# Performance work log

Measured on AMD Instinct MI355X. Metric: run time of the kernel, lower is better.

The kernel has to match this reference:

```python
import jax, jax.numpy as jnp
import numpy as np

N, E = 50000, 800000
IN_DIM, HID, HEADS, NUM_CLASSES, NUM_GRAPHS, NUM_LAYERS = 64, 64, 4, 10000, 256, 3
OUT_W = HID * HEADS  # 256


def _gat_layer(x, src, dst, W, a_src, a_dst, b, n_nodes):
    # x: [N, in], W: [heads*out, in], a_src/a_dst: [heads, out], b: [heads*out]
    h = (x @ W.T).reshape(n_nodes, HEADS, HID)            # [N, H, D]
    s_src = jnp.einsum('nhd,hd->nh', h, a_src)            # [N, H]
    s_dst = jnp.einsum('nhd,hd->nh', h, a_dst)
    alpha = jax.nn.leaky_relu(s_src[src] + s_dst[dst], 0.2)  # [E, H]
    m = jax.ops.segment_max(alpha, dst, num_segments=n_nodes)
    m = jnp.where(jnp.isfinite(m), m, 0.0)                # isolated-node safety
    ex = jnp.exp(alpha - m[dst])
    denom = jax.ops.segment_sum(ex, dst, num_segments=n_nodes)
    w = ex / (denom[dst] + 1e-16)                         # PyG softmax epsilon
    out = jax.ops.segment_sum(h[src] * w[:, :, None], dst, num_segments=n_nodes)
    return out.reshape(n_nodes, HEADS * HID) + b


def setup_inputs() -> dict:
    key = jax.random.key(0)
    ks = jax.random.split(key, 20)
    inp = {
        'x': jax.random.normal(ks[0], (N, IN_DIM), jnp.float32),
        'edge_index': jax.random.randint(ks[1], (2, E), 0, N, jnp.int32),
        'batch': jnp.sort(jax.random.randint(ks[2], (N,), 0, NUM_GRAPHS, jnp.int32)),
        'class_label': jax.random.randint(ks[3], (NUM_GRAPHS,), 0, NUM_CLASSES, jnp.int32),
        'emb': jax.random.normal(ks[4], (NUM_CLASSES, HID), jnp.float32),
    }
    in_dims = [IN_DIM + HID, OUT_W, OUT_W]
    for l in range(NUM_LAYERS):
        kw = jax.random.split(ks[5 + l], 4)
        d_in = in_dims[l]
        sc = 1.0 / np.sqrt(d_in)
        inp[f'W{l}'] = jax.random.uniform(kw[0], (OUT_W, d_in), jnp.float32, -sc, sc)
        inp[f'asrc{l}'] = jax.random.uniform(kw[1], (HEADS, HID), jnp.float32, -sc, sc)
        inp[f'adst{l}'] = jax.random.uniform(kw[2], (HEADS, HID), jnp.float32, -sc, sc)
        inp[f'b{l}'] = jnp.zeros((OUT_W,), jnp.float32)
    sc = 1.0 / np.sqrt(OUT_W)
    inp['cls_W'] = jax.random.uniform(ks[10], (1, OUT_W), jnp.float32, -sc, sc)
    inp['cls_b'] = jnp.zeros((1,), jnp.float32)
    return inp


def reference(x, edge_index, batch, class_label, emb,
              W0, asrc0, adst0, b0,
              W1, asrc1, adst1, b1,
              W2, asrc2, adst2, b2,
              cls_W, cls_b):
    n = x.shape[0]
    # template embedding aligned per node
    t = emb[class_label][batch]                          # [N, HID]
    h = jnp.concatenate([x, t], axis=-1)                 # [N, IN+HID]
    # PyG GATConv adds self-loops by default
    loop = jnp.arange(n, dtype=edge_index.dtype)
    src = jnp.concatenate([edge_index[0], loop])
    dst = jnp.concatenate([edge_index[1], loop])
    params = [(W0, asrc0, adst0, b0), (W1, asrc1, adst1, b1), (W2, asrc2, adst2, b2)]
    for (W, a_s, a_d, b) in params:
        h = _gat_layer(h, src, dst, W, a_s, a_d, b, n)
        h = jax.nn.leaky_relu(h, 0.01)                   # F.leaky_relu default slope
    return h @ cls_W.T + cls_b                           # [N, 1]
```

## Files before the change

### kernel.cpp

```cpp
#include <hip/hip_runtime.h>
#include <hip/hip_fp16.h>
#include <math.h>
#include <stdint.h>

#define NNODES 50000
#define NEDGES 800000
#define NT_TILES (((NNODES + 127) / 128) * 2)
#define NAGG_BLOCKS 2048
#define NAGG_WAVES (NAGG_BLOCKS * 4)
#define NH0 (NNODES * 128)
#define NH04 (NH0 / 4)
#define NW4 (163840 / 4)
#define NDEG4 (NNODES / 4)
#define NPREP4 (NH04 + NW4 + NDEG4)

typedef __attribute__((ext_vector_type(8))) _Float16 f16x8;
typedef __attribute__((ext_vector_type(4))) _Float16 f16x4;
typedef __attribute__((ext_vector_type(4))) float f32x4;

static __device__ __forceinline__ void gl_lds16(const void* g, void* l) {
    __builtin_amdgcn_global_load_lds(
        (const __attribute__((address_space(1))) void*)g,
        (__attribute__((address_space(3))) void*)l, 16, 0, 0);
}

static __device__ __forceinline__ float sel4(float4 v, int head) {
    float r = v.x;
    r = (head == 1) ? v.y : r;
    r = (head == 2) ? v.z : r;
    r = (head == 3) ? v.w : r;
    return r;
}

__global__ void prep_kernel(const float* __restrict__ x,
                            const int* __restrict__ batch,
                            const int* __restrict__ class_label,
                            const float* __restrict__ emb,
                            const float* __restrict__ W0,
                            const float* __restrict__ W1,
                            const float* __restrict__ W2,
                            _Float16* __restrict__ h0,
                            _Float16* __restrict__ F0,
                            _Float16* __restrict__ F1,
                            _Float16* __restrict__ F2,
                            int* __restrict__ deg) {
    int i4 = blockIdx.x * blockDim.x + threadIdx.x;
    if (i4 < NH04) {
        int idx = i4 * 4;
        int n = idx >> 7, c = idx & 127;
        float4 v;
        if (c < 64) v = *(const float4*)&x[(n << 6) + c];
        else        v = *(const float4*)&emb[class_label[batch[n]] * 64 + (c - 64)];
        f16x4 h = {(_Float16)v.x, (_Float16)v.y, (_Float16)v.z, (_Float16)v.w};
        *(f16x4*)&h0[idx] = h;
    } else if (i4 < NH04 + NW4) {
        int i = (i4 - NH04) * 4;
        const float* src; _Float16* dst;
        if (i < 32768)       { src = W0 + i;           dst = F0 + i; }
        else if (i < 98304)  { src = W1 + (i - 32768); dst = F1 + (i - 32768); }
        else                 { src = W2 + (i - 98304); dst = F2 + (i - 98304); }
        float4 v = *(const float4*)src;
        f16x4 h = {(_Float16)v.x, (_Float16)v.y, (_Float16)v.z, (_Float16)v.w};
        *(f16x4*)dst = h;
    } else if (i4 < NPREP4) {
        int j = (i4 - NH04 - NW4) * 4;
        int4 z = {0, 0, 0, 0};
        *(int4*)&deg[j] = z;
    }
}

template <int K>
static __device__ void gemm_tile_dev(const _Float16* __restrict__ A,
                                     const _Float16* __restrict__ W,
                                     const float* __restrict__ a_src,
                                     const float* __restrict__ a_dst,
                                     _Float16* __restrict__ Cf,
                                     float* __restrict__ ssrc,
                                     float* __restrict__ sdst,
                                     char* smem, int bm, int bn) {
    const int M = NNODES;
    int tid = threadIdx.x;
    int lane = tid & 63, wave = tid >> 6;
    int wm = wave >> 1, wn = wave & 1;
    int l16 = lane & 15, quad = lane >> 4;
    int rsub = lane >> 3;
    int kcs = (lane & 7) ^ rsub;
    int sw = l16 & 7;

    f32x4 acc[4][4];
#pragma unroll
    for (int r = 0; r < 4; ++r)
#pragma unroll
        for (int c = 0; c < 4; ++c) acc[r][c] = (f32x4){0.f, 0.f, 0.f, 0.f};

    const int NST = K / 64;
    auto issue = [&](int buf, int s) {
        _Float16* dA = (_Float16*)(smem + buf * 32768);
        _Float16* dB = (_Float16*)(smem + buf * 32768 + 16384);
        int ks = s * 64;
#pragma unroll
        for (int j = 0; j < 4; ++j) {
            int seg = wave * 4 + j;
            int r = seg * 8 + rsub;
            int acol = ks + kcs * 8;
            int garow = bm + r; if (garow > M - 1) garow = M - 1;
            gl_lds16(A + (size_t)garow * K + acol, &dA[seg * 512]);
            gl_lds16(W + (size_t)(bn + r) * K + acol, &dB[seg * 512]);
        }
    };

    issue(0, 0);
    __syncthreads();
#pragma unroll
    for (int s = 0; s < NST; ++s) {
        if (s + 1 < NST) issue((s + 1) & 1, s + 1);
        const _Float16* sA = (const _Float16*)(smem + (s & 1) * 32768);
        const _Float16* sB = (const _Float16*)(smem + (s & 1) * 32768 + 16384);
#pragma unroll
        for (int ks32 = 0; ks32 < 2; ++ks32) {
            f16x8 af[4], bf[4];
#pragma unroll
            for (int r = 0; r < 4; ++r) {
                int row = wm * 64 + r * 16 + l16;
                af[r] = *(const f16x8*)&sA[row * 64 + ((ks32 * 4 + quad) ^ sw) * 8];
            }
#pragma unroll
            for (int c = 0; c < 4; ++c) {
                int row = wn * 64 + c * 16 + l16;
                bf[c] = *(const f16x8*)&sB[row * 64 + ((ks32 * 4 + quad) ^ sw) * 8];
            }
#pragma unroll
            for (int r = 0; r < 4; ++r)
#pragma unroll
                for (int c = 0; c < 4; ++c)
                    acc[r][c] = __builtin_amdgcn_mfma_f32_16x16x32_f16(
                        bf[c], af[r], acc[r][c], 0, 0, 0);
        }
        __syncthreads();
    }

    int headblk = (bn + wn * 64) >> 6;
    f32x4 av[4], dv[4];
#pragma unroll
    for (int c = 0; c < 4; ++c) {
        av[c] = *(const f32x4*)&a_src[headblk * 64 + c * 16 + quad * 4];
        dv[c] = *(const f32x4*)&a_dst[headblk * 64 + c * 16 + quad * 4];
    }
#pragma unroll
    for (int r = 0; r < 4; ++r) {
        int grow = bm + wm * 64 + r * 16 + l16;
        bool ok = grow < M;
        float ps = 0.f, pd = 0.f;
#pragma unroll
        for (int c = 0; c < 4; ++c) {
            f32x4 a = acc[r][c];
            ps += a[0] * av[c][0] + a[1] * av[c][1]
                + a[2] * av[c][2] + a[3] * av[c][3];
            pd += a[0] * dv[c][0] + a[1] * dv[c][1]
                + a[2] * dv[c][2] + a[3] * dv[c][3];
            if (ok) {
                f16x4 hv = {(_Float16)a[0], (_Float16)a[1],
                            (_Float16)a[2], (_Float16)a[3]};
                *(f16x4*)&Cf[(size_t)grow * 256 + bn + wn * 64 + c * 16 + quad * 4] = hv;
            }
        }
        ps += __shfl_xor(ps, 16, 64);
        ps += __shfl_xor(ps, 32, 64);
        pd += __shfl_xor(pd, 16, 64);
        pd += __shfl_xor(pd, 32, 64);
        if (quad == 0 && ok) {
            ssrc[grow * 4 + headblk] = ps;
            sdst[grow * 4 + headblk] = pd;
        }
    }
}

template <int K>
__global__ __launch_bounds__(256) void gemm_mfma_kernel(
        const _Float16* __restrict__ A, const _Float16* __restrict__ W,
        const float* __restrict__ a_src, const float* __restrict__ a_dst,
        _Float16* __restrict__ Cf,
        float* __restrict__ ssrc, float* __restrict__ sdst) {
    __shared__ __align__(16) char smem[65536];
    gemm_tile_dev<K>(A, W, a_src, a_dst, Cf, ssrc, sdst, smem,
                     blockIdx.x * 128, blockIdx.y * 128);
}

__global__ __launch_bounds__(256) void gemm0_bucket_kernel(
        const _Float16* __restrict__ A, const _Float16* __restrict__ W,
        const float* __restrict__ a_src, const float* __restrict__ a_dst,
        _Float16* __restrict__ Cf,
        float* __restrict__ ssrc, float* __restrict__ sdst,
        const int* __restrict__ ei,
        int* __restrict__ deg, int* __restrict__ slots) {
    __shared__ __align__(16) char smem[65536];
    int b = blockIdx.x;
    if ((b & 1) == 0) {
        int tile = b >> 1;
        if (tile < NT_TILES)
            gemm_tile_dev<128>(A, W, a_src, a_dst, Cf, ssrc, sdst, smem,
                               (tile >> 1) * 128, (tile & 1) * 128);
    } else {
        int rel = b >> 1;
        int stride = NT_TILES * 256;
        for (int e = rel * 256 + (int)threadIdx.x; e < NEDGES; e += stride) {
            int d = ei[NEDGES + e];
            int pos = atomicAdd(&deg[d], 1);
            if (pos < 64) slots[(size_t)d * 64 + pos] = ei[e] << 9;
        }
    }
}

template <bool LAST>
__global__ __launch_bounds__(256) void aggregate_kernel(
        const _Float16* __restrict__ hpf,
        const float* __restrict__ ssrc,
        const float* __restrict__ sdst,
        const int* __restrict__ deg,
        const int* __restrict__ slots,
        const float* __restrict__ bias,
        _Float16* __restrict__ out_h,
        const float* __restrict__ cls_W,
        const float* __restrict__ cls_b,
        float* __restrict__ out) {
    __shared__ __align__(16) float s_w[4][64][4];
    __shared__ int s_idx[4][64];
    int lane = threadIdx.x & 63;
    int slot = threadIdx.x >> 6;
    int wid = blockIdx.x * 4 + slot;
    int head = lane >> 4;
    uint32_t lane8 = (uint32_t)lane * 8u;
    const char* hbase = (const char*)hpf;

    float4 bv = ((const float4*)bias)[lane];
    float4 wv = LAST ? ((const float4*)cls_W)[lane] : (float4){0.f, 0.f, 0.f, 0.f};

    for (int n = wid; n < NNODES; n += NAGG_WAVES) {
        int dn = deg[n]; if (dn > 64) dn = 64;
        float4 sd = ((const float4*)sdst)[n];

        float4 ssl = ((const float4*)ssrc)[n];
        float ax = ssl.x + sd.x, ay = ssl.y + sd.y;
        float az = ssl.z + sd.z, aw = ssl.w + sd.w;
        ax = ax > 0.f ? ax : 0.2f * ax;
        ay = ay > 0.f ? ay : 0.2f * ay;
        az = az > 0.f ? az : 0.2f * az;
        aw = aw > 0.f ? aw : 0.2f * aw;
        float4 exs = {__expf(ax), __expf(ay), __expf(az), __expf(aw)};
        float wself = sel4(exs, head);
        f16x4 vs = *(const f16x4*)(hbase + (((uint32_t)n << 9) + lane8));
        float dsum = wself;
        float4 acc = {wself * (float)vs.x, wself * (float)vs.y,
                      wself * (float)vs.z, wself * (float)vs.w};

        float4 ex = {0.f, 0.f, 0.f, 0.f};
        int soff = 0;
        if (lane < dn) {
            soff = slots[(size_t)n * 64 + lane];
            float4 ss = *(const float4*)((const char*)ssrc + ((uint32_t)soff >> 5));
            float bx = ss.x + sd.x, by = ss.y + sd.y;
            float bz = ss.z + sd.z, bw = ss.w + sd.w;
            bx = bx > 0.f ? bx : 0.2f * bx;
            by = by > 0.f ? by : 0.2f * by;
            bz = bz > 0.f ? bz : 0.2f * bz;
            bw = bw > 0.f ? bw : 0.2f * bw;
            ex.x = __expf(bx); ex.y = __expf(by);
            ex.z = __expf(bz); ex.w = __expf(bw);
        }
        *(float4*)&s_w[slot][lane][0] = ex;
        s_idx[slot][lane] = soff;

        int e = 0;
        for (; e + 8 <= dn; e += 8) {
            int si[8]; float w[8]; f16x4 v[8];
#pragma unroll
            for (int t = 0; t < 8; ++t) {
                si[t] = s_idx[slot][e + t];
                w[t] = s_w[slot][e + t][head];
            }
#pragma unroll
            for (int t = 0; t < 8; ++t)
                v[t] = *(const f16x4*)(hbase + ((uint32_t)si[t] + lane8));
#pragma unroll
            for (int t = 0; t < 8; ++t) {
                dsum += w[t];
                acc.x += w[t] * (float)v[t].x;
                acc.y += w[t] * (float)v[t].y;
                acc.z += w[t] * (float)v[t].z;
                acc.w += w[t] * (float)v[t].w;
            }
        }
        for (; e < dn; ++e) {
            int si = s_idx[slot][e];
            float w = s_w[slot][e][head];
            f16x4 v = *(const f16x4*)(hbase + ((uint32_t)si + lane8));
            dsum += w;
            acc.x += w * (float)v.x; acc.y += w * (float)v.y;
            acc.z += w * (float)v.z; acc.w += w * (float)v.w;
        }

        float inv = 1.f / (dsum + 1e-16f);
        float4 o;
        o.x = acc.x * inv + bv.x;
        o.y = acc.y * inv + bv.y;
        o.z = acc.z * inv + bv.z;
        o.w = acc.w * inv + bv.w;
        o.x = o.x > 0.f ? o.x : 0.01f * o.x;
        o.y = o.y > 0.f ? o.y : 0.01f * o.y;
        o.z = o.z > 0.f ? o.z : 0.01f * o.z;
        o.w = o.w > 0.f ? o.w : 0.01f * o.w;

        if (!LAST) {
            f16x4 ov = {(_Float16)o.x, (_Float16)o.y, (_Float16)o.z, (_Float16)o.w};
            ((f16x4*)out_h)[(size_t)n * 64 + lane] = ov;
        } else {
            float sdot = o.x * wv.x + o.y * wv.y + o.z * wv.z + o.w * wv.w;
#pragma unroll
            for (int off = 1; off < 64; off <<= 1)
                sdot += __shfl_xor(sdot, off, 64);
            if (lane == 0) out[n] = sdot + cls_b[0];
        }
    }
}

extern "C" void kernel_launch(void* const* d_in, const int* in_sizes, int n_in,
                              void* d_out, int out_size, void* d_ws, size_t ws_size,
                              hipStream_t stream) {
    const float* x     = (const float*)d_in[0];
    const int*   ei    = (const int*)d_in[1];
    const int*   batch = (const int*)d_in[2];
    const int*   clab  = (const int*)d_in[3];
    const float* emb   = (const float*)d_in[4];
    const float* W[3]    = {(const float*)d_in[5], (const float*)d_in[9],  (const float*)d_in[13]};
    const float* asrc[3] = {(const float*)d_in[6], (const float*)d_in[10], (const float*)d_in[14]};
    const float* adst[3] = {(const float*)d_in[7], (const float*)d_in[11], (const float*)d_in[15]};
    const float* bias[3] = {(const float*)d_in[8], (const float*)d_in[12], (const float*)d_in[16]};
    const float* clsW = (const float*)d_in[17];
    const float* clsb = (const float*)d_in[18];
    float* out = (float*)d_out;

    char* ws = (char*)d_ws;
    size_t off = 0;
    auto alloc = [&](size_t bytes) {
        void* p = ws + off;
        off += (bytes + 255) & ~(size_t)255;
        return p;
    };
    _Float16* Cf   = (_Float16*)alloc((size_t)NNODES * 256 * 2);
    _Float16* hA   = (_Float16*)alloc((size_t)NNODES * 256 * 2);
    _Float16* h0f  = (_Float16*)alloc((size_t)NNODES * 128 * 2);
    _Float16* Wf[3];
    Wf[0] = (_Float16*)alloc((size_t)256 * 128 * 2);
    Wf[1] = (_Float16*)alloc((size_t)256 * 256 * 2);
    Wf[2] = (_Float16*)alloc((size_t)256 * 256 * 2);
    float* ssrc  = (float*)alloc((size_t)NNODES * 4 * 4);
    float* sdst  = (float*)alloc((size_t)NNODES * 4 * 4);
    int*   deg   = (int*)alloc((size_t)NNODES * 4);
    int*   slots = (int*)alloc((size_t)NNODES * 64 * 4);
    (void)ws_size; (void)in_sizes; (void)n_in; (void)out_size;

    prep_kernel<<<dim3((NPREP4 + 255) / 256), dim3(256), 0, stream>>>(
        x, batch, clab, emb, W[0], W[1], W[2], h0f, Wf[0], Wf[1], Wf[2], deg);

    dim3 gemm_grid((NNODES + 127) / 128, 2);
    dim3 node_grid(NAGG_BLOCKS);

    gemm0_bucket_kernel<<<dim3(NT_TILES * 2), dim3(256), 0, stream>>>(
        h0f, Wf[0], asrc[0], adst[0], Cf, ssrc, sdst, ei, deg, slots);
    aggregate_kernel<false><<<node_grid, dim3(256), 0, stream>>>(
        Cf, ssrc, sdst, deg, slots, bias[0], hA, nullptr, nullptr, nullptr);

    gemm_mfma_kernel<256><<<gemm_grid, dim3(256), 0, stream>>>(
        hA, Wf[1], asrc[1], adst[1], Cf, ssrc, sdst);
    aggregate_kernel<false><<<node_grid, dim3(256), 0, stream>>>(
        Cf, ssrc, sdst, deg, slots, bias[1], hA, nullptr, nullptr, nullptr);

    gemm_mfma_kernel<256><<<gemm_grid, dim3(256), 0, stream>>>(
        hA, Wf[2], asrc[2], adst[2], Cf, ssrc, sdst);
    aggregate_kernel<true><<<node_grid, dim3(256), 0, stream>>>(
        Cf, ssrc, sdst, deg, slots, bias[2], nullptr, clsW, clsb, out);
}
```

Measured before the change: 384.0 us.

## Use atomic work-stealing queues over node ranges in aggregate kernel

After: 852.9 us. +122.1%, slower.

```diff
diff --git a/kernel.cpp b/kernel.cpp
--- a/kernel.cpp
+++ b/kernel.cpp
@@ -7,12 +7,14 @@
 #define NEDGES 800000
 #define NT_TILES (((NNODES + 127) / 128) * 2)
 #define NAGG_BLOCKS 2048
-#define NAGG_WAVES (NAGG_BLOCKS * 4)
+#define NRANGE 6250
+#define QCHUNK 4
 #define NH0 (NNODES * 128)
 #define NH04 (NH0 / 4)
 #define NW4 (163840 / 4)
 #define NDEG4 (NNODES / 4)
-#define NPREP4 (NH04 + NW4 + NDEG4)
+#define NCTR4 96
+#define NPREP4 (NH04 + NW4 + NDEG4 + NCTR4)
 
 typedef __attribute__((ext_vector_type(8))) _Float16 f16x8;
 typedef __attribute__((ext_vector_type(4))) _Float16 f16x4;
@@ -43,7 +45,8 @@
                             _Float16* __restrict__ F0,
                             _Float16* __restrict__ F1,
                             _Float16* __restrict__ F2,
-                            int* __restrict__ deg) {
+                            int* __restrict__ deg,
+                            int* __restrict__ ctr) {
     int i4 = blockIdx.x * blockDim.x + threadIdx.x;
     if (i4 < NH04) {
         int idx = i4 * 4;
@@ -62,10 +65,14 @@
         float4 v = *(const float4*)src;
         f16x4 h = {(_Float16)v.x, (_Float16)v.y, (_Float16)v.z, (_Float16)v.w};
         *(f16x4*)dst = h;
-    } else if (i4 < NPREP4) {
+    } else if (i4 < NH04 + NW4 + NDEG4) {
         int j = (i4 - NH04 - NW4) * 4;
         int4 z = {0, 0, 0, 0};
         *(int4*)&deg[j] = z;
+    } else if (i4 < NPREP4) {
+        int j = (i4 - NH04 - NW4 - NDEG4) * 4;
+        int4 z = {0, 0, 0, 0};
+        *(int4*)&ctr[j] = z;
     }
 }
 
@@ -222,7 +229,8 @@
         _Float16* __restrict__ out_h,
         const float* __restrict__ cls_W,
         const float* __restrict__ cls_b,
-        float* __restrict__ out) {
+        float* __restrict__ out,
+        int* __restrict__ ctr) {
     __shared__ __align__(16) float s_w[4][64][4];
     __shared__ int s_idx[4][64];
     int lane = threadIdx.x & 63;
@@ -234,91 +242,106 @@
 
     float4 bv = ((const float4*)bias)[lane];
     float4 wv = LAST ? ((const float4*)cls_W)[lane] : (float4){0.f, 0.f, 0.f, 0.f};
-
-    for (int n = wid; n < NNODES; n += NAGG_WAVES) {
-        int dn = deg[n]; if (dn > 64) dn = 64;
-        float4 sd = ((const float4*)sdst)[n];
-
-        float4 ssl = ((const float4*)ssrc)[n];
-        float ax = ssl.x + sd.x, ay = ssl.y + sd.y;
-        float az = ssl.z + sd.z, aw = ssl.w + sd.w;
-        ax = ax > 0.f ? ax : 0.2f * ax;
-        ay = ay > 0.f ? ay : 0.2f * ay;
-        az = az > 0.f ? az : 0.2f * az;
-        aw = aw > 0.f ? aw : 0.2f * aw;
-        float4 exs = {__expf(ax), __expf(ay), __expf(az), __expf(aw)};
-        float wself = sel4(exs, head);
-        f16x4 vs = *(const f16x4*)(hbase + (((uint32_t)n << 9) + lane8));
-        float dsum = wself;
-        float4 acc = {wself * (float)vs.x, wself * (float)vs.y,
-                      wself * (float)vs.z, wself * (float)vs.w};
-
-        float4 ex = {0.f, 0.f, 0.f, 0.f};
-        int soff = 0;
-        if (lane < dn) {
-            soff = slots[(size_t)n * 64 + lane];
-            float4 ss = *(const float4*)((const char*)ssrc + ((uint32_t)soff >> 5));
-            float bx = ss.x + sd.x, by = ss.y + sd.y;
-            float bz = ss.z + sd.z, bw = ss.w + sd.w;
-            bx = bx > 0.f ? bx : 0.2f * bx;
-            by = by > 0.f ? by : 0.2f * by;
-            bz = bz > 0.f ? bz : 0.2f * bz;
-            bw = bw > 0.f ? bw : 0.2f * bw;
-            ex.x = __expf(bx); ex.y = __expf(by);
-            ex.z = __expf(bz); ex.w = __expf(bw);
-        }
-        *(float4*)&s_w[slot][lane][0] = ex;
-        s_idx[slot][lane] = soff;
-
-        int e = 0;
-        for (; e + 8 <= dn; e += 8) {
-            int si[8]; float w[8]; f16x4 v[8];
-#pragma unroll
-            for (int t = 0; t < 8; ++t) {
-                si[t] = s_idx[slot][e + t];
-                w[t] = s_w[slot][e + t][head];
+    float cb = 0.f;
+    if (LAST) cb = cls_b[0];
+
+    int g0 = wid & 7;
+    for (int k = 0; k < 8; ++k) {
+        int g = (g0 + k) & 7;
+        int rbase = g * NRANGE;
+        for (;;) {
+            int b0 = 0;
+            if (lane == 0) b0 = atomicAdd(&ctr[g * 16], QCHUNK);
+            b0 = __shfl(b0, 0, 64);
+            if (b0 >= NRANGE) break;
+            int n1 = rbase + b0 + QCHUNK;
+            for (int n = rbase + b0; n < n1; ++n) {
+                int dn = deg[n]; if (dn > 64) dn = 64;
+                float4 sd = ((const float4*)sdst)[n];
+
+                float4 ssl = ((const float4*)ssrc)[n];
+                float ax = ssl.x + sd.x, ay = ssl.y + sd.y;
+                float az = ssl.z + sd.z, aw = ssl.w + sd.w;
+                ax = ax > 0.f ? ax : 0.2f * ax;
+                ay = ay > 0.f ? ay : 0.2f * ay;
+                az = az > 0.f ? az : 0.2f * az;
+                aw = aw > 0.f ? aw : 0.2f * aw;
+                float4 exs = {__expf(ax), __expf(ay), __expf(az), __expf(aw)};
+                float wself = sel4(exs, head);
+                f16x4 vs = *(const f16x4*)(hbase + (((uint32_t)n << 9) + lane8));
+                float dsum = wself;
+                float4 acc = {wself * (float)vs.x, wself * (float)vs.y,
+                              wself * (float)vs.z, wself * (float)vs.w};
+
+                float4 ex = {0.f, 0.f, 0.f, 0.f};
+                int soff = 0;
+                if (lane < dn) {
+                    soff = slots[(size_t)n * 64 + lane];
+                    float4 ss = *(const float4*)((const char*)ssrc + ((uint32_t)soff >> 5));
+                    float bx = ss.x + sd.x, by = ss.y + sd.y;
+                    float bz = ss.z + sd.z, bw = ss.w + sd.w;
+                    bx = bx > 0.f ? bx : 0.2f * bx;
+                    by = by > 0.f ? by : 0.2f * by;
+                    bz = bz > 0.f ? bz : 0.2f * bz;
+                    bw = bw > 0.f ? bw : 0.2f * bw;
+                    ex.x = __expf(bx); ex.y = __expf(by);
+                    ex.z = __expf(bz); ex.w = __expf(bw);
+                }
+                *(float4*)&s_w[slot][lane][0] = ex;
+                s_idx[slot][lane] = soff;
+
+                int e = 0;
+                for (; e + 8 <= dn; e += 8) {
+                    int si[8]; float w[8]; f16x4 v[8];
+#pragma unroll
+                    for (int t = 0; t < 8; ++t) {
+                        si[t] = s_idx[slot][e + t];
+                        w[t] = s_w[slot][e + t][head];
+                    }
+#pragma unroll
+                    for (int t = 0; t < 8; ++t)
+                        v[t] = *(const f16x4*)(hbase + ((uint32_t)si[t] + lane8));
+#pragma unroll
+                    for (int t = 0; t < 8; ++t) {
+                        dsum += w[t];
+                        acc.x += w[t] * (float)v[t].x;
+                        acc.y += w[t] * (float)v[t].y;
+                        acc.z += w[t] * (float)v[t].z;
+                        acc.w += w[t] * (float)v[t].w;
+                    }
+                }
+                for (; e < dn; ++e) {
+                    int si = s_idx[slot][e];
+                    float w = s_w[slot][e][head];
+                    f16x4 v = *(const f16x4*)(hbase + ((uint32_t)si + lane8));
+                    dsum += w;
+                    acc.x += w * (float)v.x; acc.y += w * (float)v.y;
+                    acc.z += w * (float)v.z; acc.w += w * (float)v.w;
+                }
+
+                float inv = 1.f / (dsum + 1e-16f);
+                float4 o;
+                o.x = acc.x * inv + bv.x;
+                o.y = acc.y * inv + bv.y;
+                o.z = acc.z * inv + bv.z;
+                o.w = acc.w * inv + bv.w;
+                o.x = o.x > 0.f ? o.x : 0.01f * o.x;
+                o.y = o.y > 0.f ? o.y : 0.01f * o.y;
+                o.z = o.z > 0.f ? o.z : 0.01f * o.z;
+                o.w = o.w > 0.f ? o.w : 0.01f * o.w;
+
+                if (!LAST) {
+                    f16x4 ov = {(_Float16)o.x, (_Float16)o.y,
+                                (_Float16)o.z, (_Float16)o.w};
+                    ((f16x4*)out_h)[(size_t)n * 64 + lane] = ov;
+                } else {
+                    float sdot = o.x * wv.x + o.y * wv.y + o.z * wv.z + o.w * wv.w;
+#pragma unroll
+                    for (int off = 1; off < 64; off <<= 1)
+                        sdot += __shfl_xor(sdot, off, 64);
+                    if (lane == 0) out[n] = sdot + cb;
+                }
             }
-#pragma unroll
-            for (int t = 0; t < 8; ++t)
-                v[t] = *(const f16x4*)(hbase + ((uint32_t)si[t] + lane8));
-#pragma unroll
-            for (int t = 0; t < 8; ++t) {
-                dsum += w[t];
-                acc.x += w[t] * (float)v[t].x;
-                acc.y += w[t] * (float)v[t].y;
-                acc.z += w[t] * (float)v[t].z;
-                acc.w += w[t] * (float)v[t].w;
-            }
-        }
-        for (; e < dn; ++e) {
-            int si = s_idx[slot][e];
-            float w = s_w[slot][e][head];
-            f16x4 v = *(const f16x4*)(hbase + ((uint32_t)si + lane8));
-            dsum += w;
-            acc.x += w * (float)v.x; acc.y += w * (float)v.y;
-            acc.z += w * (float)v.z; acc.w += w * (float)v.w;
-        }
-
-        float inv = 1.f / (dsum + 1e-16f);
-        float4 o;
-        o.x = acc.x * inv + bv.x;
-        o.y = acc.y * inv + bv.y;
-        o.z = acc.z * inv + bv.z;
-        o.w = acc.w * inv + bv.w;
-        o.x = o.x > 0.f ? o.x : 0.01f * o.x;
-        o.y = o.y > 0.f ? o.y : 0.01f * o.y;
-        o.z = o.z > 0.f ? o.z : 0.01f * o.z;
-        o.w = o.w > 0.f ? o.w : 0.01f * o.w;
-
-        if (!LAST) {
-            f16x4 ov = {(_Float16)o.x, (_Float16)o.y, (_Float16)o.z, (_Float16)o.w};
-            ((f16x4*)out_h)[(size_t)n * 64 + lane] = ov;
-        } else {
-            float sdot = o.x * wv.x + o.y * wv.y + o.z * wv.z + o.w * wv.w;
-#pragma unroll
-            for (int off = 1; off < 64; off <<= 1)
-                sdot += __shfl_xor(sdot, off, 64);
-            if (lane == 0) out[n] = sdot + cls_b[0];
         }
     }
 }
@@ -357,10 +380,11 @@
     float* sdst  = (float*)alloc((size_t)NNODES * 4 * 4);
     int*   deg   = (int*)alloc((size_t)NNODES * 4);
     int*   slots = (int*)alloc((size_t)NNODES * 64 * 4);
+    int*   ctr   = (int*)alloc((size_t)3 * 128 * 4);
     (void)ws_size; (void)in_sizes; (void)n_in; (void)out_size;
 
     prep_kernel<<<dim3((NPREP4 + 255) / 256), dim3(256), 0, stream>>>(
-        x, batch, clab, emb, W[0], W[1], W[2], h0f, Wf[0], Wf[1], Wf[2], deg);
+        x, batch, clab, emb, W[0], W[1], W[2], h0f, Wf[0], Wf[1], Wf[2], deg, ctr);
 
     dim3 gemm_grid((NNODES + 127) / 128, 2);
     dim3 node_grid(NAGG_BLOCKS);
@@ -368,15 +392,15 @@
     gemm0_bucket_kernel<<<dim3(NT_TILES * 2), dim3(256), 0, stream>>>(
         h0f, Wf[0], asrc[0], adst[0], Cf, ssrc, sdst, ei, deg, slots);
     aggregate_kernel<false><<<node_grid, dim3(256), 0, stream>>>(
-        Cf, ssrc, sdst, deg, slots, bias[0], hA, nullptr, nullptr, nullptr);
+        Cf, ssrc, sdst, deg, slots, bias[0], hA, nullptr, nullptr, nullptr, ctr);
 
     gemm_mfma_kernel<256><<<gemm_grid, dim3(256), 0, stream>>>(
         hA, Wf[1], asrc[1], adst[1], Cf, ssrc, sdst);
     aggregate_kernel<false><<<node_grid, dim3(256), 0, stream>>>(
-        Cf, ssrc, sdst, deg, slots, bias[1], hA, nullptr, nullptr, nullptr);
+        Cf, ssrc, sdst, deg, slots, bias[1], hA, nullptr, nullptr, nullptr, ctr + 128);
 
     gemm_mfma_kernel<256><<<gemm_grid, dim3(256), 0, stream>>>(
         hA, Wf[2], asrc[2], adst[2], Cf, ssrc, sdst);
     aggregate_kernel<true><<<node_grid, dim3(256), 0, stream>>>(
-        Cf, ssrc, sdst, deg, slots, bias[2], nullptr, clsW, clsb, out);
-}
+        Cf, ssrc, sdst, deg, slots, bias[2], nullptr, clsW, clsb, out, ctr + 256);
+}
```
